# Kernel optimization log

Hardware: AMD Instinct MI355X
Metric: run time of the kernel (lower is better)

Reference implementation:

```python
import jax, jax.numpy as jnp
import numpy as np

B, T, C = 2, 512, 128
H = 4 * C
EPS_LN = 1e-5
EPS_WKV = 1e-6


def setup_inputs() -> dict:
    key = jax.random.key(0)
    ks = jax.random.split(key, 12)
    def rn(i, shape, s):
        return jax.random.normal(ks[i], shape, jnp.float32) * s
    return {
        "x": jax.random.normal(ks[0], (B, T, C), jnp.float32),
        "ln1_g": jnp.ones((C,), jnp.float32), "ln1_b": jnp.zeros((C,), jnp.float32),
        "mu": rn(1, (C,), 0.1),
        "Wr": rn(2, (C, C), 0.02), "br": jnp.zeros((C,), jnp.float32),
        "Wk": rn(3, (C, C), 0.02), "bk": jnp.zeros((C,), jnp.float32),
        "Wv": rn(4, (C, C), 0.02), "bv": jnp.zeros((C,), jnp.float32),
        "w_decay": rn(5, (C,), 0.5),
        "Wo": rn(6, (C, C), 0.02), "bo": jnp.zeros((C,), jnp.float32),
        "ln2_g": jnp.ones((C,), jnp.float32), "ln2_b": jnp.zeros((C,), jnp.float32),
        "W1": rn(7, (C, H), 0.02), "b1": jnp.zeros((H,), jnp.float32),
        "W2": rn(8, (H, C), 0.02), "b2": jnp.zeros((C,), jnp.float32),
    }


def _ln(x, g, b):
    m = x.mean(-1, keepdims=True)
    v = ((x - m) ** 2).mean(-1, keepdims=True)
    return (x - m) * jax.lax.rsqrt(v + EPS_LN) * g + b


def _wkv_dir(k, v, w_lc):
    # k, v: (B,T,C); w_lc: (T,C) per-(position,channel) decay weight
    p = k[:, :, None, :] * w_lc[None, None, :, :]              # (B,T,L,C)
    p = jnp.exp(p - jax.lax.stop_gradient(p.max(-1, keepdims=True)))  # stable, max over C (as in source, dim=-1)
    p = p / (p.sum(-1, keepdims=True) + EPS_WKV)               # normalize over channel dim, as written in torch
    return jnp.einsum('btlc,blc->btc', p, v)


def _forward(x, ln1_g, ln1_b, mu, Wr, br, Wk, bk, Wv, bv, w_decay, Wo, bo, ln2_g, ln2_b, W1, b1, W2, b2):
    Tn = x.shape[1]
    h = _ln(x, ln1_g, ln1_b)
    # TemporalShift: past half shifted right, future half shifted left
    xp, xf = jnp.split(h, 2, axis=-1)
    xp = jnp.pad(xp, ((0, 0), (1, 0), (0, 0)))[:, :-1]
    xf = jnp.pad(xf, ((0, 0), (0, 1), (0, 0)))[:, 1:]
    hs = h + mu * jnp.concatenate([xp, xf], axis=-1)
    r = jax.nn.sigmoid(hs @ Wr + br)
    k = hs @ Wk + bk
    v = hs @ Wv + bv
    t = jnp.arange(Tn, dtype=x.dtype)[:, None]                 # (T,1)
    neg_w = -jnp.exp(w_decay)[None, :]                         # (1,C)
    w_f = neg_w * (Tn - 1 - t) / (Tn - 1)                      # (T,C)
    w_b = neg_w * t / (Tn - 1)                                 # (T,C)
    x_f = _wkv_dir(k, v, w_f)
    x_b = jnp.flip(_wkv_dir(jnp.flip(k, 1), jnp.flip(v, 1), w_b), 1)
    wk = r * (x_f + x_b) * 0.5
    y = x + wk @ Wo + bo
    h2 = _ln(y, ln2_g, ln2_b)
    m = jax.nn.gelu(h2 @ W1 + b1, approximate=False) @ W2 + b2
    return y + m


def reference(x, ln1_g, ln1_b, mu, Wr, br, Wk, bk, Wv, bv, w_decay, Wo, bo, ln2_g, ln2_b, W1, b1, W2, b2):
    return _forward(x, ln1_g, ln1_b, mu, Wr, br, Wk, bk, Wv, bv, w_decay, Wo, bo, ln2_g, ln2_b, W1, b1, W2, b2)
```

## Files before the change

### kernel.cpp

```cpp
#include <hip/hip_runtime.h>
#include <hip/hip_bf16.h>

#define Bq 2
#define Tq 512
#define Cq 128
#define Hq 512
#define NROW (Bq*Tq)

__device__ __forceinline__ float bf2f(__hip_bfloat16 v) { return __bfloat162float(v); }

__device__ __forceinline__ bool detect_f32(const void* sent) {
    return *(const unsigned*)sent == 0x3F800000u;
}

#define LD(p, i) (f32 ? ((const float*)(p))[i] : bf2f(((const __hip_bfloat16*)(p))[i]))

__global__ __launch_bounds__(128) void k1_ln1(
    const void* __restrict__ x,
    const void* __restrict__ g,
    const void* __restrict__ b,
    float* __restrict__ h)
{
    const bool f32 = detect_f32(g);
    int row = blockIdx.x, tid = threadIdx.x;
    float xv = LD(x, row * Cq + tid);
    float s1 = xv, s2 = xv * xv;
    for (int off = 32; off; off >>= 1) {
        s1 += __shfl_xor(s1, off);
        s2 += __shfl_xor(s2, off);
    }
    __shared__ float wred[2][2];
    int wid = tid >> 6;
    if ((tid & 63) == 0) { wred[wid][0] = s1; wred[wid][1] = s2; }
    __syncthreads();
    float S1 = wred[0][0] + wred[1][0];
    float S2 = wred[0][1] + wred[1][1];
    float m  = S1 * (1.f / Cq);
    float va = S2 * (1.f / Cq) - m * m;
    float rs = rsqrtf(va + 1e-5f);
    h[row * Cq + tid] = (xv - m) * rs * LD(g, tid) + LD(b, tid);
}

__global__ __launch_bounds__(384) void k2_qkv(
    const void* __restrict__ sent,
    const float* __restrict__ h,
    const void* __restrict__ mu,
    const void* __restrict__ Wr, const void* __restrict__ br,
    const void* __restrict__ Wk, const void* __restrict__ bk,
    const void* __restrict__ Wv, const void* __restrict__ bv,
    const void* __restrict__ wdec,
    float* __restrict__ r_out, float* __restrict__ u_out,
    float* __restrict__ v_out)
{
    const bool f32 = detect_f32(sent);
    int R0 = blockIdx.x * 2, tid = threadIdx.x;
    int g = tid >> 7, col = tid & 127;
    int t0 = R0 & (Tq - 1);
    __shared__ float hs2[2][Cq];
    if (g == 0) {
        float muv = LD(mu, col);
#pragma unroll
        for (int r2 = 0; r2 < 2; ++r2) {
            int row = R0 + r2, t = t0 + r2;
            float hv = h[row * Cq + col];
            float nb;
            if (col < Cq / 2) nb = (t > 0)      ? h[(row - 1) * Cq + col] : 0.f;
            else              nb = (t < Tq - 1) ? h[(row + 1) * Cq + col] : 0.f;
            hs2[r2][col] = hv + muv * nb;
        }
    }
    __syncthreads();
    const void* W = (g == 0) ? Wr : (g == 1) ? Wk : Wv;
    float a0 = 0.f, a1 = 0.f;
    for (int cc = 0; cc < Cq; cc += 4) {
        float w0 = LD(W, (cc + 0) * Cq + col);
        float w1 = LD(W, (cc + 1) * Cq + col);
        float w2 = LD(W, (cc + 2) * Cq + col);
        float w3 = LD(W, (cc + 3) * Cq + col);
        a0 += hs2[0][cc] * w0;     a1 += hs2[1][cc] * w0;
        a0 += hs2[0][cc + 1] * w1; a1 += hs2[1][cc + 1] * w1;
        a0 += hs2[0][cc + 2] * w2; a1 += hs2[1][cc + 2] * w2;
        a0 += hs2[0][cc + 3] * w3; a1 += hs2[1][cc + 3] * w3;
    }
    if (g == 0) {
        float brv = LD(br, col);
        float r0 = 1.f / (1.f + __expf(-(a0 + brv)));
        float r1 = 1.f / (1.f + __expf(-(a1 + brv)));
        r_out[(R0 + 0) * Cq + col] = r0;
        r_out[(R0 + 1) * Cq + col] = r1;
    } else if (g == 1) {
        float bkv = LD(bk, col);
        float wd = LD(wdec, col);
        wd = fminf(fmaxf(wd, -20.f), 20.f);
        float negw = -__expf(wd);
        float u0 = (a0 + bkv) * negw;
        float u1 = (a1 + bkv) * negw;
        u0 = fminf(fmaxf(u0, -30.f), 30.f);
        u1 = fminf(fmaxf(u1, -30.f), 30.f);
        u_out[(R0 + 0) * Cq + col] = u0;
        u_out[(R0 + 1) * Cq + col] = u1;
    } else {
        float bvv = LD(bv, col);
        v_out[(R0 + 0) * Cq + col] = a0 + bvv;
        v_out[(R0 + 1) * Cq + col] = a1 + bvv;
    }
}

__global__ __launch_bounds__(512) void k3_wkv(
    const void* __restrict__ sent,
    const float* __restrict__ u_in,
    const float* __restrict__ v_in,
    const float* __restrict__ r_in,
    const void* __restrict__ x,
    const void* __restrict__ Wo, const void* __restrict__ bo,
    float* __restrict__ y_out)
{
    const bool f32 = detect_f32(sent);
    int row = blockIdx.x, tid = threadIdx.x;
    int b = row >> 9;
    int c = tid & 127, seg = tid >> 7;
    __shared__ float u_l[Cq];
    __shared__ float rinv_l[Tq];
    __shared__ float wk_l[Cq];
    __shared__ float part[4][Cq];
    __shared__ float part2[4][Cq];
    if (tid < Cq) u_l[tid] = u_in[row * Cq + tid];
    __syncthreads();

    const float inv511 = 1.f / (float)(Tq - 1);
    {
        int l = tid;
        float a = (float)(Tq - 1 - l) * inv511 * 1.44269504f;
        float s0 = 0.f, s1 = 0.f, s2 = 0.f, s3 = 0.f;
        const float4* u4 = (const float4*)u_l;
        for (int cc = 0; cc < Cq / 4; ++cc) {
            float4 uv = u4[cc];
            s0 += exp2f(a * uv.x);
            s1 += exp2f(a * uv.y);
            s2 += exp2f(a * uv.z);
            s3 += exp2f(a * uv.w);
        }
        rinv_l[l] = 1.f / ((s0 + s1) + (s2 + s3) + 1e-6f);
    }
    __syncthreads();

    float uu = u_l[c];
    float g1 = __expf(uu * inv511);
    float g2 = g1 * g1, g3 = g2 * g1, g4 = g2 * g2;
    float e = __expf(uu * (float)(seg * 128) * inv511);
    float a0 = 0.f, a1 = 0.f, a2 = 0.f, a3 = 0.f;
    const float* vb = v_in + (size_t)b * Tq * Cq + c;
    int j0 = seg * 128;
    for (int j = j0; j < j0 + 128; j += 4) {
        int l = (Tq - 1) - j;
        a0 += vb[l * Cq]       * (e        * rinv_l[l]);
        a1 += vb[(l - 1) * Cq] * ((e * g1) * rinv_l[l - 1]);
        a2 += vb[(l - 2) * Cq] * ((e * g2) * rinv_l[l - 2]);
        a3 += vb[(l - 3) * Cq] * ((e * g3) * rinv_l[l - 3]);
        e *= g4;
    }
    part[seg][c] = (a0 + a1) + (a2 + a3);
    __syncthreads();
    if (tid < Cq) {
        float acc = (part[0][tid] + part[1][tid]) + (part[2][tid] + part[3][tid]);
        wk_l[tid] = r_in[row * Cq + tid] * acc;
    }
    __syncthreads();

    {
        float s = 0.f;
        int c0 = seg * 32;
#pragma unroll 4
        for (int cc = c0; cc < c0 + 32; ++cc) s += wk_l[cc] * LD(Wo, cc * Cq + c);
        part2[seg][c] = s;
    }
    __syncthreads();
    if (tid < Cq)
        y_out[row * Cq + tid] = LD(x, row * Cq + tid)
            + ((part2[0][tid] + part2[1][tid]) + (part2[2][tid] + part2[3][tid]))
            + LD(bo, tid);
}

__global__ __launch_bounds__(512) void k4_ffn(
    const void* __restrict__ sent,
    const float* __restrict__ y_in,
    const void* __restrict__ lng, const void* __restrict__ lnb,
    const void* __restrict__ W1, const void* __restrict__ b1,
    const void* __restrict__ W2, const void* __restrict__ b2,
    void* __restrict__ out)
{
    const bool f32 = detect_f32(sent);
    int R0 = blockIdx.x * 2, tid = threadIdx.x;
    __shared__ float h2s[2][Cq];
    __shared__ float m1s[2][Hq];
    __shared__ float part[4][2][Cq];
    __shared__ float wred[8][2];
    int r2 = (tid >> 7) & 1, c = tid & 127;
    float yv = 0.f;
    if (tid < 256) yv = y_in[(R0 + r2) * Cq + c];
    float s1 = yv, s2 = yv * yv;
    for (int off = 32; off; off >>= 1) {
        s1 += __shfl_xor(s1, off);
        s2 += __shfl_xor(s2, off);
    }
    int wid = tid >> 6;
    if ((tid & 63) == 0) { wred[wid][0] = s1; wred[wid][1] = s2; }
    __syncthreads();
    if (tid < 256) {
        int w0 = r2 << 1;
        float S1 = wred[w0][0] + wred[w0 + 1][0];
        float S2 = wred[w0][1] + wred[w0 + 1][1];
        float m  = S1 * (1.f / Cq);
        float va = S2 * (1.f / Cq) - m * m;
        float rs = rsqrtf(va + 1e-5f);
        h2s[r2][c] = (yv - m) * rs * LD(lng, c) + LD(lnb, c);
    }
    __syncthreads();

    {
        int j = tid;
        float a0 = 0.f, a1 = 0.f;
        for (int cc = 0; cc < Cq; cc += 4) {
            float w0 = LD(W1, (cc + 0) * Hq + j);
            float w1 = LD(W1, (cc + 1) * Hq + j);
            float w2 = LD(W1, (cc + 2) * Hq + j);
            float w3 = LD(W1, (cc + 3) * Hq + j);
            a0 += h2s[0][cc] * w0;     a1 += h2s[1][cc] * w0;
            a0 += h2s[0][cc + 1] * w1; a1 += h2s[1][cc + 1] * w1;
            a0 += h2s[0][cc + 2] * w2; a1 += h2s[1][cc + 2] * w2;
            a0 += h2s[0][cc + 3] * w3; a1 += h2s[1][cc + 3] * w3;
        }
        float bb = LD(b1, j);
        float x0 = a0 + bb, x1 = a1 + bb;
        m1s[0][j] = 0.5f * x0 * (1.f + erff(x0 * 0.70710678f));
        m1s[1][j] = 0.5f * x1 * (1.f + erff(x1 * 0.70710678f));
    }
    __syncthreads();

    {
        int kseg = tid >> 7;
        int h0 = kseg * 128;
        float a0 = 0.f, a1 = 0.f;
        for (int hh = h0; hh < h0 + 128; hh += 4) {
            float w0 = LD(W2, (hh + 0) * Cq + c);
            float w1 = LD(W2, (hh + 1) * Cq + c);
            float w2 = LD(W2, (hh + 2) * Cq + c);
            float w3 = LD(W2, (hh + 3) * Cq + c);
            a0 += m1s[0][hh] * w0;     a1 += m1s[1][hh] * w0;
            a0 += m1s[0][hh + 1] * w1; a1 += m1s[1][hh + 1] * w1;
            a0 += m1s[0][hh + 2] * w2; a1 += m1s[1][hh + 2] * w2;
            a0 += m1s[0][hh + 3] * w3; a1 += m1s[1][hh + 3] * w3;
        }
        part[kseg][0][c] = a0;
        part[kseg][1][c] = a1;
    }
    __syncthreads();
    if (tid < 256) {
        float s = ((part[0][r2][c] + part[1][r2][c]) + (part[2][r2][c] + part[3][r2][c]));
        float val = yv + s + LD(b2, c);
        int idx = (R0 + r2) * Cq + c;
        if (f32) ((float*)out)[idx] = val;
        else     ((__hip_bfloat16*)out)[idx] = __float2bfloat16(val);
    }
}

extern "C" void kernel_launch(void* const* d_in, const int* in_sizes, int n_in,
                              void* d_out, int out_size, void* d_ws, size_t ws_size,
                              hipStream_t stream)
{
    const void* x    = d_in[0];
    const void* ln1g = d_in[1];
    const void* ln1b = d_in[2];
    const void* mu   = d_in[3];
    const void* Wr   = d_in[4];
    const void* br   = d_in[5];
    const void* Wk   = d_in[6];
    const void* bk   = d_in[7];
    const void* Wv   = d_in[8];
    const void* bv   = d_in[9];
    const void* wdec = d_in[10];
    const void* Wo   = d_in[11];
    const void* bo   = d_in[12];
    const void* ln2g = d_in[13];
    const void* ln2b = d_in[14];
    const void* W1   = d_in[15];
    const void* b1   = d_in[16];
    const void* W2   = d_in[17];
    const void* b2   = d_in[18];

    float* ws = (float*)d_ws;
    float* h  = ws;
    float* u  = ws + 131072;
    float* r  = ws + 262144;
    float* y  = ws + 393216;
    float* v  = ws + 524288;

    k1_ln1<<<NROW,     128, 0, stream>>>(x, ln1g, ln1b, h);
    k2_qkv<<<NROW / 2, 384, 0, stream>>>(ln1g, h, mu, Wr, br, Wk, bk, Wv, bv, wdec, r, u, v);
    k3_wkv<<<NROW,     512, 0, stream>>>(ln1g, u, v, r, x, Wo, bo, y);
    k4_ffn<<<NROW / 2, 512, 0, stream>>>(ln1g, y, ln2g, ln2b, W1, b1, W2, b2, d_out);
}
```

Before: 154.7 us.

## Fuse LN1 into QKV kernel and vectorize WKV and FFN inner loops

Removes the separate LayerNorm kernel: each QKV block recomputes LN for its two rows plus neighbours, then splits the K dimension across four thread groups computing r, k and v together, followed by a shared-memory reduction. The WKV kernel processes two channels per thread with float2/float4 loads over eight sequence segments. The FFN first matmul becomes a K-split with float4 weight loads and a reduction, and the second matmul is unrolled by eight with vector LDS reads. This saves one launch and the h round trip at the cost of redundant LN work and extra shared memory.

After: 153.8 us. No clear change (-0.5%).

```diff
diff --git a/kernel.cpp b/kernel.cpp
--- a/kernel.cpp
+++ b/kernel.cpp
@@ -7,43 +7,23 @@
 #define Hq 512
 #define NROW (Bq*Tq)
 
-__device__ __forceinline__ float bf2f(__hip_bfloat16 v) { return __bfloat162float(v); }
-
+__device__ __forceinline__ float bfbits2f(unsigned short u) {
+    return __uint_as_float(((unsigned)u) << 16);
+}
 __device__ __forceinline__ bool detect_f32(const void* sent) {
     return *(const unsigned*)sent == 0x3F800000u;
 }
-
-#define LD(p, i) (f32 ? ((const float*)(p))[i] : bf2f(((const __hip_bfloat16*)(p))[i]))
-
-__global__ __launch_bounds__(128) void k1_ln1(
+#define LD(p, i) (f32 ? ((const float*)(p))[i] : bfbits2f(((const unsigned short*)(p))[i]))
+__device__ __forceinline__ float4 LD4(const void* p, int i, bool f32) {
+    if (f32) return ((const float4*)p)[i >> 2];
+    ushort4 u = *(const ushort4*)((const unsigned short*)p + i);
+    return make_float4(bfbits2f(u.x), bfbits2f(u.y), bfbits2f(u.z), bfbits2f(u.w));
+}
+
+__global__ __launch_bounds__(512) void k2_qkv(
+    const void* __restrict__ sent,
     const void* __restrict__ x,
-    const void* __restrict__ g,
-    const void* __restrict__ b,
-    float* __restrict__ h)
-{
-    const bool f32 = detect_f32(g);
-    int row = blockIdx.x, tid = threadIdx.x;
-    float xv = LD(x, row * Cq + tid);
-    float s1 = xv, s2 = xv * xv;
-    for (int off = 32; off; off >>= 1) {
-        s1 += __shfl_xor(s1, off);
-        s2 += __shfl_xor(s2, off);
-    }
-    __shared__ float wred[2][2];
-    int wid = tid >> 6;
-    if ((tid & 63) == 0) { wred[wid][0] = s1; wred[wid][1] = s2; }
-    __syncthreads();
-    float S1 = wred[0][0] + wred[1][0];
-    float S2 = wred[0][1] + wred[1][1];
-    float m  = S1 * (1.f / Cq);
-    float va = S2 * (1.f / Cq) - m * m;
-    float rs = rsqrtf(va + 1e-5f);
-    h[row * Cq + tid] = (xv - m) * rs * LD(g, tid) + LD(b, tid);
-}
-
-__global__ __launch_bounds__(384) void k2_qkv(
-    const void* __restrict__ sent,
-    const float* __restrict__ h,
+    const void* __restrict__ ln1g, const void* __restrict__ ln1b,
     const void* __restrict__ mu,
     const void* __restrict__ Wr, const void* __restrict__ br,
     const void* __restrict__ Wk, const void* __restrict__ bk,
@@ -56,53 +36,103 @@
     int R0 = blockIdx.x * 2, tid = threadIdx.x;
     int g = tid >> 7, col = tid & 127;
     int t0 = R0 & (Tq - 1);
+    int bbase = R0 - t0;
+
+    __shared__ float h4[4][Cq];
     __shared__ float hs2[2][Cq];
-    if (g == 0) {
-        float muv = LD(mu, col);
+    __shared__ float part[4][6][Cq];
+    __shared__ float wred[8][2];
+
+    {
+        int t = t0 - 1 + g;
+        int tcl = min(max(t, 0), Tq - 1);
+        int row = bbase + tcl;
+        float xv = LD(x, row * Cq + col);
+        float s1 = xv, s2 = xv * xv;
+        for (int off = 32; off; off >>= 1) {
+            s1 += __shfl_xor(s1, off);
+            s2 += __shfl_xor(s2, off);
+        }
+        int wid = tid >> 6;
+        if ((tid & 63) == 0) { wred[wid][0] = s1; wred[wid][1] = s2; }
+        __syncthreads();
+        float S1 = wred[2 * g][0] + wred[2 * g + 1][0];
+        float S2 = wred[2 * g][1] + wred[2 * g + 1][1];
+        float m  = S1 * (1.f / Cq);
+        float va = S2 * (1.f / Cq) - m * m;
+        float rs = rsqrtf(va + 1e-5f);
+        h4[g][col] = (xv - m) * rs * LD(ln1g, col) + LD(ln1b, col);
+    }
+    __syncthreads();
+
+    if (g < 2) {
+        int r2 = g, tt = t0 + r2;
+        float hv = h4[r2 + 1][col];
+        float nb;
+        if (col < Cq / 2) nb = (tt > 0)      ? h4[r2][col]     : 0.f;
+        else              nb = (tt < Tq - 1) ? h4[r2 + 2][col] : 0.f;
+        hs2[r2][col] = hv + LD(mu, col) * nb;
+    }
+    __syncthreads();
+
+    {
+        float ar0 = 0.f, ar1 = 0.f, ak0 = 0.f, ak1 = 0.f, av0 = 0.f, av1 = 0.f;
+        int c0 = g * 32;
+        for (int cc = c0; cc < c0 + 32; cc += 4) {
+            float4 h0 = *(const float4*)&hs2[0][cc];
+            float4 h1 = *(const float4*)&hs2[1][cc];
+            float wr0 = LD(Wr, (cc + 0) * Cq + col);
+            float wr1 = LD(Wr, (cc + 1) * Cq + col);
+            float wr2 = LD(Wr, (cc + 2) * Cq + col);
+            float wr3 = LD(Wr, (cc + 3) * Cq + col);
+            float wk0 = LD(Wk, (cc + 0) * Cq + col);
+            float wk1 = LD(Wk, (cc + 1) * Cq + col);
+            float wk2 = LD(Wk, (cc + 2) * Cq + col);
+            float wk3 = LD(Wk, (cc + 3) * Cq + col);
+            float wv0 = LD(Wv, (cc + 0) * Cq + col);
+            float wv1 = LD(Wv, (cc + 1) * Cq + col);
+            float wv2 = LD(Wv, (cc + 2) * Cq + col);
+            float wv3 = LD(Wv, (cc + 3) * Cq + col);
+            ar0 += h0.x * wr0; ar1 += h1.x * wr0;
+            ak0 += h0.x * wk0; ak1 += h1.x * wk0;
+            av0 += h0.x * wv0; av1 += h1.x * wv0;
+            ar0 += h0.y * wr1; ar1 += h1.y * wr1;
+            ak0 += h0.y * wk1; ak1 += h1.y * wk1;
+            av0 += h0.y * wv1; av1 += h1.y * wv1;
+            ar0 += h0.z * wr2; ar1 += h1.z * wr2;
+            ak0 += h0.z * wk2; ak1 += h1.z * wk2;
+            av0 += h0.z * wv2; av1 += h1.z * wv2;
+            ar0 += h0.w * wr3; ar1 += h1.w * wr3;
+            ak0 += h0.w * wk3; ak1 += h1.w * wk3;
+            av0 += h0.w * wv3; av1 += h1.w * wv3;
+        }
+        part[g][0][col] = ar0; part[g][1][col] = ar1;
+        part[g][2][col] = ak0; part[g][3][col] = ak1;
+        part[g][4][col] = av0; part[g][5][col] = av1;
+    }
+    __syncthreads();
+
+    if (g < 3) {
 #pragma unroll
         for (int r2 = 0; r2 < 2; ++r2) {
-            int row = R0 + r2, t = t0 + r2;
-            float hv = h[row * Cq + col];
-            float nb;
-            if (col < Cq / 2) nb = (t > 0)      ? h[(row - 1) * Cq + col] : 0.f;
-            else              nb = (t < Tq - 1) ? h[(row + 1) * Cq + col] : 0.f;
-            hs2[r2][col] = hv + muv * nb;
-        }
-    }
-    __syncthreads();
-    const void* W = (g == 0) ? Wr : (g == 1) ? Wk : Wv;
-    float a0 = 0.f, a1 = 0.f;
-    for (int cc = 0; cc < Cq; cc += 4) {
-        float w0 = LD(W, (cc + 0) * Cq + col);
-        float w1 = LD(W, (cc + 1) * Cq + col);
-        float w2 = LD(W, (cc + 2) * Cq + col);
-        float w3 = LD(W, (cc + 3) * Cq + col);
-        a0 += hs2[0][cc] * w0;     a1 += hs2[1][cc] * w0;
-        a0 += hs2[0][cc + 1] * w1; a1 += hs2[1][cc + 1] * w1;
-        a0 += hs2[0][cc + 2] * w2; a1 += hs2[1][cc + 2] * w2;
-        a0 += hs2[0][cc + 3] * w3; a1 += hs2[1][cc + 3] * w3;
-    }
-    if (g == 0) {
-        float brv = LD(br, col);
-        float r0 = 1.f / (1.f + __expf(-(a0 + brv)));
-        float r1 = 1.f / (1.f + __expf(-(a1 + brv)));
-        r_out[(R0 + 0) * Cq + col] = r0;
-        r_out[(R0 + 1) * Cq + col] = r1;
-    } else if (g == 1) {
-        float bkv = LD(bk, col);
-        float wd = LD(wdec, col);
-        wd = fminf(fmaxf(wd, -20.f), 20.f);
-        float negw = -__expf(wd);
-        float u0 = (a0 + bkv) * negw;
-        float u1 = (a1 + bkv) * negw;
-        u0 = fminf(fmaxf(u0, -30.f), 30.f);
-        u1 = fminf(fmaxf(u1, -30.f), 30.f);
-        u_out[(R0 + 0) * Cq + col] = u0;
-        u_out[(R0 + 1) * Cq + col] = u1;
-    } else {
-        float bvv = LD(bv, col);
-        v_out[(R0 + 0) * Cq + col] = a0 + bvv;
-        v_out[(R0 + 1) * Cq + col] = a1 + bvv;
+            int m = 2 * g + r2;
+            float a = (part[0][m][col] + part[1][m][col])
+                    + (part[2][m][col] + part[3][m][col]);
+            int row = R0 + r2;
+            if (g == 0) {
+                float rr = 1.f / (1.f + __expf(-(a + LD(br, col))));
+                r_out[row * Cq + col] = rr;
+            } else if (g == 1) {
+                float wd = LD(wdec, col);
+                wd = fminf(fmaxf(wd, -20.f), 20.f);
+                float negw = -__expf(wd);
+                float uu = (a + LD(bk, col)) * negw;
+                uu = fminf(fmaxf(uu, -30.f), 30.f);
+                u_out[row * Cq + col] = uu;
+            } else {
+                v_out[row * Cq + col] = a + LD(bv, col);
+            }
+        }
     }
 }
 
@@ -118,11 +148,10 @@
     const bool f32 = detect_f32(sent);
     int row = blockIdx.x, tid = threadIdx.x;
     int b = row >> 9;
-    int c = tid & 127, seg = tid >> 7;
     __shared__ float u_l[Cq];
     __shared__ float rinv_l[Tq];
     __shared__ float wk_l[Cq];
-    __shared__ float part[4][Cq];
+    __shared__ float part[8][Cq];
     __shared__ float part2[4][Cq];
     if (tid < Cq) u_l[tid] = u_in[row * Cq + tid];
     __syncthreads();
@@ -144,35 +173,57 @@
     }
     __syncthreads();
 
-    float uu = u_l[c];
-    float g1 = __expf(uu * inv511);
-    float g2 = g1 * g1, g3 = g2 * g1, g4 = g2 * g2;
-    float e = __expf(uu * (float)(seg * 128) * inv511);
-    float a0 = 0.f, a1 = 0.f, a2 = 0.f, a3 = 0.f;
-    const float* vb = v_in + (size_t)b * Tq * Cq + c;
-    int j0 = seg * 128;
-    for (int j = j0; j < j0 + 128; j += 4) {
-        int l = (Tq - 1) - j;
-        a0 += vb[l * Cq]       * (e        * rinv_l[l]);
-        a1 += vb[(l - 1) * Cq] * ((e * g1) * rinv_l[l - 1]);
-        a2 += vb[(l - 2) * Cq] * ((e * g2) * rinv_l[l - 2]);
-        a3 += vb[(l - 3) * Cq] * ((e * g3) * rinv_l[l - 3]);
-        e *= g4;
-    }
-    part[seg][c] = (a0 + a1) + (a2 + a3);
+    {
+        int cidx = tid & 63, seg = tid >> 6;
+        int c2 = cidx * 2;
+        float2 uu = *(const float2*)&u_l[c2];
+        float g1x = __expf(uu.x * inv511),      g1y = __expf(uu.y * inv511);
+        float g2x = g1x * g1x,                  g2y = g1y * g1y;
+        float g3x = g2x * g1x,                  g3y = g2y * g1y;
+        float g4x = g2x * g2x,                  g4y = g2y * g2y;
+        float jb  = (float)(seg * 64);
+        float ex  = __expf(uu.x * jb * inv511), ey = __expf(uu.y * jb * inv511);
+        float a0x = 0.f, a0y = 0.f, a1x = 0.f, a1y = 0.f;
+        float a2x = 0.f, a2y = 0.f, a3x = 0.f, a3y = 0.f;
+        const float2* vb2 = (const float2*)(v_in + (size_t)b * Tq * Cq) + cidx;
+        int j0 = seg * 64;
+        for (int j = j0; j < j0 + 64; j += 4) {
+            int l = (Tq - 1) - j;
+            float4 rv = *(const float4*)&rinv_l[l - 3];
+            float2 v0 = vb2[(size_t)l * 64];
+            float2 v1 = vb2[(size_t)(l - 1) * 64];
+            float2 v2 = vb2[(size_t)(l - 2) * 64];
+            float2 v3 = vb2[(size_t)(l - 3) * 64];
+            a0x += v0.x * (ex * rv.w);          a0y += v0.y * (ey * rv.w);
+            a1x += v1.x * ((ex * g1x) * rv.z);  a1y += v1.y * ((ey * g1y) * rv.z);
+            a2x += v2.x * ((ex * g2x) * rv.y);  a2y += v2.y * ((ey * g2y) * rv.y);
+            a3x += v3.x * ((ex * g3x) * rv.x);  a3y += v3.y * ((ey * g3y) * rv.x);
+            ex *= g4x; ey *= g4y;
+        }
+        float px = (a0x + a1x) + (a2x + a3x);
+        float py = (a0y + a1y) + (a2y + a3y);
+        *(float2*)&part[seg][c2] = make_float2(px, py);
+    }
     __syncthreads();
     if (tid < Cq) {
-        float acc = (part[0][tid] + part[1][tid]) + (part[2][tid] + part[3][tid]);
+        float acc = ((part[0][tid] + part[1][tid]) + (part[2][tid] + part[3][tid]))
+                  + ((part[4][tid] + part[5][tid]) + (part[6][tid] + part[7][tid]));
         wk_l[tid] = r_in[row * Cq + tid] * acc;
     }
     __syncthreads();
 
     {
+        int seg4 = tid >> 7, c = tid & 127;
         float s = 0.f;
-        int c0 = seg * 32;
-#pragma unroll 4
-        for (int cc = c0; cc < c0 + 32; ++cc) s += wk_l[cc] * LD(Wo, cc * Cq + c);
-        part2[seg][c] = s;
+        int c0 = seg4 * 32;
+        for (int cc = c0; cc < c0 + 32; cc += 4) {
+            float4 wv4 = *(const float4*)&wk_l[cc];
+            s += wv4.x * LD(Wo, (cc + 0) * Cq + c);
+            s += wv4.y * LD(Wo, (cc + 1) * Cq + c);
+            s += wv4.z * LD(Wo, (cc + 2) * Cq + c);
+            s += wv4.w * LD(Wo, (cc + 3) * Cq + c);
+        }
+        part2[seg4][c] = s;
     }
     __syncthreads();
     if (tid < Cq)
@@ -193,6 +244,7 @@
     int R0 = blockIdx.x * 2, tid = threadIdx.x;
     __shared__ float h2s[2][Cq];
     __shared__ float m1s[2][Hq];
+    __shared__ float part1[4][2][Hq];
     __shared__ float part[4][2][Cq];
     __shared__ float wred[8][2];
     int r2 = (tid >> 7) & 1, c = tid & 127;
@@ -218,20 +270,35 @@
     __syncthreads();
 
     {
+        int kseg = tid >> 7, j4 = (tid & 127) * 4;
+        float a00 = 0.f, a01 = 0.f, a02 = 0.f, a03 = 0.f;
+        float a10 = 0.f, a11 = 0.f, a12 = 0.f, a13 = 0.f;
+        int c0 = kseg * 32;
+        for (int cc = c0; cc < c0 + 32; cc += 4) {
+            float4 w0 = LD4(W1, (cc + 0) * Hq + j4, f32);
+            float4 w1 = LD4(W1, (cc + 1) * Hq + j4, f32);
+            float4 w2 = LD4(W1, (cc + 2) * Hq + j4, f32);
+            float4 w3 = LD4(W1, (cc + 3) * Hq + j4, f32);
+            float4 h0 = *(const float4*)&h2s[0][cc];
+            float4 h1 = *(const float4*)&h2s[1][cc];
+            a00 += h0.x * w0.x; a01 += h0.x * w0.y; a02 += h0.x * w0.z; a03 += h0.x * w0.w;
+            a10 += h1.x * w0.x; a11 += h1.x * w0.y; a12 += h1.x * w0.z; a13 += h1.x * w0.w;
+            a00 += h0.y * w1.x; a01 += h0.y * w1.y; a02 += h0.y * w1.z; a03 += h0.y * w1.w;
+            a10 += h1.y * w1.x; a11 += h1.y * w1.y; a12 += h1.y * w1.z; a13 += h1.y * w1.w;
+            a00 += h0.z * w2.x; a01 += h0.z * w2.y; a02 += h0.z * w2.z; a03 += h0.z * w2.w;
+            a10 += h1.z * w2.x; a11 += h1.z * w2.y; a12 += h1.z * w2.z; a13 += h1.z * w2.w;
+            a00 += h0.w * w3.x; a01 += h0.w * w3.y; a02 += h0.w * w3.z; a03 += h0.w * w3.w;
+            a10 += h1.w * w3.x; a11 += h1.w * w3.y; a12 += h1.w * w3.z; a13 += h1.w * w3.w;
+        }
+        *(float4*)&part1[kseg][0][j4] = make_float4(a00, a01, a02, a03);
+        *(float4*)&part1[kseg][1][j4] = make_float4(a10, a11, a12, a13);
+    }
+    __syncthreads();
+    {
         int j = tid;
-        float a0 = 0.f, a1 = 0.f;
-        for (int cc = 0; cc < Cq; cc += 4) {
-            float w0 = LD(W1, (cc + 0) * Hq + j);
-            float w1 = LD(W1, (cc + 1) * Hq + j);
-            float w2 = LD(W1, (cc + 2) * Hq + j);
-            float w3 = LD(W1, (cc + 3) * Hq + j);
-            a0 += h2s[0][cc] * w0;     a1 += h2s[1][cc] * w0;
-            a0 += h2s[0][cc + 1] * w1; a1 += h2s[1][cc + 1] * w1;
-            a0 += h2s[0][cc + 2] * w2; a1 += h2s[1][cc + 2] * w2;
-            a0 += h2s[0][cc + 3] * w3; a1 += h2s[1][cc + 3] * w3;
-        }
         float bb = LD(b1, j);
-        float x0 = a0 + bb, x1 = a1 + bb;
+        float x0 = ((part1[0][0][j] + part1[1][0][j]) + (part1[2][0][j] + part1[3][0][j])) + bb;
+        float x1 = ((part1[0][1][j] + part1[1][1][j]) + (part1[2][1][j] + part1[3][1][j])) + bb;
         m1s[0][j] = 0.5f * x0 * (1.f + erff(x0 * 0.70710678f));
         m1s[1][j] = 0.5f * x1 * (1.f + erff(x1 * 0.70710678f));
     }
@@ -241,15 +308,27 @@
         int kseg = tid >> 7;
         int h0 = kseg * 128;
         float a0 = 0.f, a1 = 0.f;
-        for (int hh = h0; hh < h0 + 128; hh += 4) {
+        for (int hh = h0; hh < h0 + 128; hh += 8) {
+            float4 ma = *(const float4*)&m1s[0][hh];
+            float4 mb = *(const float4*)&m1s[0][hh + 4];
+            float4 na = *(const float4*)&m1s[1][hh];
+            float4 nb = *(const float4*)&m1s[1][hh + 4];
             float w0 = LD(W2, (hh + 0) * Cq + c);
             float w1 = LD(W2, (hh + 1) * Cq + c);
             float w2 = LD(W2, (hh + 2) * Cq + c);
             float w3 = LD(W2, (hh + 3) * Cq + c);
-            a0 += m1s[0][hh] * w0;     a1 += m1s[1][hh] * w0;
-            a0 += m1s[0][hh + 1] * w1; a1 += m1s[1][hh + 1] * w1;
-            a0 += m1s[0][hh + 2] * w2; a1 += m1s[1][hh + 2] * w2;
-            a0 += m1s[0][hh + 3] * w3; a1 += m1s[1][hh + 3] * w3;
+            float w4 = LD(W2, (hh + 4) * Cq + c);
+            float w5 = LD(W2, (hh + 5) * Cq + c);
+            float w6 = LD(W2, (hh + 6) * Cq + c);
+            float w7 = LD(W2, (hh + 7) * Cq + c);
+            a0 += ma.x * w0; a1 += na.x * w0;
+            a0 += ma.y * w1; a1 += na.y * w1;
+            a0 += ma.z * w2; a1 += na.z * w2;
+            a0 += ma.w * w3; a1 += na.w * w3;
+            a0 += mb.x * w4; a1 += nb.x * w4;
+            a0 += mb.y * w5; a1 += nb.y * w5;
+            a0 += mb.z * w6; a1 += nb.z * w6;
+            a0 += mb.w * w7; a1 += nb.w * w7;
         }
         part[kseg][0][c] = a0;
         part[kseg][1][c] = a1;
@@ -289,14 +368,12 @@
     const void* b2   = d_in[18];
 
     float* ws = (float*)d_ws;
-    float* h  = ws;
-    float* u  = ws + 131072;
-    float* r  = ws + 262144;
-    float* y  = ws + 393216;
-    float* v  = ws + 524288;
-
-    k1_ln1<<<NROW,     128, 0, stream>>>(x, ln1g, ln1b, h);
-    k2_qkv<<<NROW / 2, 384, 0, stream>>>(ln1g, h, mu, Wr, br, Wk, bk, Wv, bv, wdec, r, u, v);
+    float* u  = ws;
+    float* r  = ws + 131072;
+    float* y  = ws + 262144;
+    float* v  = ws + 393216;
+
+    k2_qkv<<<NROW / 2, 512, 0, stream>>>(ln1g, x, ln1g, ln1b, mu, Wr, br, Wk, bk, Wv, bv, wdec, r, u, v);
     k3_wkv<<<NROW,     512, 0, stream>>>(ln1g, u, v, r, x, Wo, bo, y);
     k4_ffn<<<NROW / 2, 512, 0, stream>>>(ln1g, y, ln2g, ln2b, W1, b1, W2, b2, d_out);
 }
```
